# Optimization experiments

Hardware: AMD Instinct MI355X
Metric: run time of the kernel (lower is better)

Reference implementation:

```python
import jax, jax.numpy as jnp
import numpy as np

NEG = -10000.0
LN_EPS = 1e-5


def _longformer_attn(x, attn_val, Wq, bq, Wk, bk, Wv, bv, Wqg, bqg, Wkg, bkg, Wvg, bvg, w, H):
    # x: (B, S, D) with S % (2w) == 0; attn_val: (B, S) int, 0=local, -1=pad, +1=global (only last pos)
    B, S, D = x.shape
    d = D // H
    scale = float(1.0 / np.sqrt(d))
    q = (x @ Wq + bq).reshape(B, S, H, d) * scale
    k = (x @ Wk + bk).reshape(B, S, H, d)
    v = (x @ Wv + bv).reshape(B, S, H, d)
    g = S - 1                      # single global token (last position)
    C = S // w                     # number of query chunks of size w
    W3 = 3 * w
    # key/value windows: chunk c sees absolute keys [c*w - w, c*w + 2w)
    idx = np.arange(C)[:, None] * w + np.arange(W3)[None, :]           # (C, 3w) into padded length S+2w
    k_win = jnp.pad(k, ((0, 0), (w, w), (0, 0), (0, 0)))[:, idx]       # (B, C, 3w, H, d)
    v_win = jnp.pad(v, ((0, 0), (w, w), (0, 0), (0, 0)))[:, idx]
    qc = q.reshape(B, C, w, H, d)
    scores = jnp.einsum('bcxhd,bcyhd->bhcxy', qc, k_win)               # (B, H, C, w, 3w)
    # banded validity: relative offset in [-w, w] and absolute key index in [0, S)
    x_i = np.arange(w)[:, None]
    y_i = np.arange(W3)[None, :]
    rel_ok = (y_i - x_i >= 0) & (y_i - x_i <= 2 * w)                   # (w, 3w)
    j_abs = np.arange(C)[:, None, None] * w - w + y_i[None]            # (C, 1, 3w)
    valid = jnp.asarray(rel_ok[None] & ((j_abs >= 0) & (j_abs < S)))   # (C, w, 3w)
    # keys that are padding or global get -10000 inside the band (remove_from_windowed_attention_mask)
    rm_win = jnp.pad(attn_val != 0, ((0, 0), (w, w)))[:, idx]          # (B, C, 3w)
    scores = scores + jnp.where(rm_win, NEG, 0.0)[:, None, :, None, :]
    scores = jnp.where(valid[None, None], scores, -jnp.inf)
    # every query also attends to the global key (column prepended before softmax)
    g_scores = jnp.einsum('bcxhd,bhd->bhcx', qc, k[:, g])              # (B, H, C, w)
    all_s = jnp.concatenate([g_scores[..., None], scores], axis=-1)    # (B, H, C, w, 3w+1)
    probs = jax.nn.softmax(all_s, axis=-1)
    q_ok = (attn_val >= 0).astype(probs.dtype)                         # zero rows of padding queries
    probs = probs * q_ok.reshape(B, 1, C, w, 1)
    out = jnp.einsum('bhcxy,bcyhd->bcxhd', probs[..., 1:], v_win)
    out = out + jnp.einsum('bhcx,bhd->bcxhd', probs[..., 0], v[:, g])
    out = out.reshape(B, S, D)
    # global token: full attention over all keys with the *_global projections
    qg = (x[:, g] @ Wqg + bqg).reshape(B, H, d) * scale
    kg = (x @ Wkg + bkg).reshape(B, S, H, d)
    vg = (x @ Wvg + bvg).reshape(B, S, H, d)
    sg = jnp.einsum('bhd,bshd->bhs', qg, kg)
    sg = sg + jnp.where(attn_val < 0, NEG, 0.0)[:, None, :]
    og = jnp.einsum('bhs,bshd->bhd', jax.nn.softmax(sg, axis=-1), vg).reshape(B, D)
    return out.at[:, g].set(og)


def setup_inputs() -> dict:
    B, S, D, H, w, E = 2, 2048, 768, 12, 256, 4
    key = jax.random.key(0)
    ks = jax.random.split(key, 16)
    wmat = lambda k, s: jax.random.normal(k, s, dtype=jnp.float32) * 0.02
    inp = {
        'x': jax.random.normal(ks[0], (B, S, D), dtype=jnp.float32),
        'mask': jnp.ones((B, S), dtype=bool),
        'Wq': wmat(ks[1], (D, D)), 'bq': jnp.zeros((D,), jnp.float32),
        'Wk': wmat(ks[2], (D, D)), 'bk': jnp.zeros((D,), jnp.float32),
        'Wv': wmat(ks[3], (D, D)), 'bv': jnp.zeros((D,), jnp.float32),
        'Wqg': wmat(ks[4], (D, D)), 'bqg': jnp.zeros((D,), jnp.float32),
        'Wkg': wmat(ks[5], (D, D)), 'bkg': jnp.zeros((D,), jnp.float32),
        'Wvg': wmat(ks[6], (D, D)), 'bvg': jnp.zeros((D,), jnp.float32),
        'ln_g': jnp.ones((D,), jnp.float32), 'ln_b': jnp.zeros((D,), jnp.float32),
        'W1': wmat(ks[7], (D, E * D)), 'b1': jnp.zeros((E * D,), jnp.float32),
        'W2': wmat(ks[8], (E * D, D)), 'b2': jnp.zeros((D,), jnp.float32),
        'window_size': w,
        'num_heads': H,
    }
    return inp


def reference(x, mask, Wq, bq, Wk, bk, Wv, bv, Wqg, bqg, Wkg, bkg, Wvg, bvg,
              ln_g, ln_b, W1, b1, W2, b2, window_size, num_heads):
    B, S0, D = x.shape
    w = int(window_size)
    H = int(num_heads)
    pad = 2 * w - S0 % (2 * w)                          # always in [1, 2w], matches torch code
    xp = jnp.pad(x, ((0, 0), (0, pad), (0, 0)))         # pad_token_id = 0
    mp = jnp.pad(mask, ((0, 0), (0, pad)), constant_values=True)
    attn_val = mp.astype(jnp.int32) - 1                 # True->0 (local), False->-1 (pad)
    attn_val = attn_val.at[:, -1].set(1)                # last position is global
    xp = xp + _longformer_attn(xp, attn_val, Wq, bq, Wk, bk, Wv, bv,
                               Wqg, bqg, Wkg, bkg, Wvg, bvg, w, H)
    x1 = xp[:, :S0]
    mu = jnp.mean(x1, axis=-1, keepdims=True)
    var = jnp.mean((x1 - mu) ** 2, axis=-1, keepdims=True)
    xn = (x1 - mu) * jax.lax.rsqrt(var + LN_EPS) * ln_g + ln_b
    h = jax.nn.gelu(xn @ W1 + b1, approximate=False)
    return xn + h @ W2 + b2
```

## Files before the change

### kernel.cpp

```cpp
#include <hip/hip_runtime.h>
#include <hip/hip_bf16.h>

typedef unsigned short ushort_t;
typedef __attribute__((ext_vector_type(8))) __bf16 bf16x8;
typedef __attribute__((ext_vector_type(4))) float f32x4;
typedef __attribute__((ext_vector_type(4))) unsigned short us4;

#define S0 2048
#define DM 768
#define NH 12
#define DH 64
#define KS 2368
#define GK 2304

__device__ __forceinline__ float bf2f(ushort_t h){
  union{unsigned u; float f;} x; x.u = ((unsigned)h)<<16; return x.f;
}
__device__ __forceinline__ ushort_t f2bf(float f){
  union{float f; unsigned u;} x; x.f = f;
  unsigned r = (x.u + 0x7FFFu + ((x.u>>16)&1u))>>16;
  return (ushort_t)r;
}

typedef void as1_void __attribute__((address_space(1)));
typedef void as3_void __attribute__((address_space(3)));
__device__ __forceinline__ void lds_cp16(const void* g, void* s){
  __builtin_amdgcn_global_load_lds((as1_void*)g, (as3_void*)s, 16, 0, 0);
}

__device__ __forceinline__ int xcd_swizzle(int bid, int nwg){
  const int q8 = nwg>>3, r8 = nwg&7;
  const int xcd = bid & 7, sub = bid >> 3;
  return (xcd < r8 ? xcd*(q8+1) : r8*(q8+1) + (xcd-r8)*q8) + sub;
}

__global__ __launch_bounds__(256)
void prep_kernel(const float* __restrict__ Wq, const float* __restrict__ Wk,
                 const float* __restrict__ Wv, const float* __restrict__ W1,
                 const float* __restrict__ W2, const float* __restrict__ x,
                 const float* __restrict__ bq, const float* __restrict__ bk,
                 const float* __restrict__ bv,
                 ushort_t* __restrict__ WtQ, ushort_t* __restrict__ WtK,
                 ushort_t* __restrict__ WtV, ushort_t* __restrict__ Wt1,
                 ushort_t* __restrict__ Wt2, ushort_t* __restrict__ xb,
                 float* __restrict__ bqkv, ushort_t* __restrict__ Kb,
                 ushort_t* __restrict__ Vtb)
{
  __shared__ ushort_t tile[64][72];
  const int id = blockIdx.x, t = threadIdx.x;
  if (id < 1584){
    const float* src; ushort_t* dst; int K, N, bx, by;
    if (id < 432){
      const int m = id/144, r = id%144;
      src = (m==0)?Wq:((m==1)?Wk:Wv);
      dst = (m==0)?WtQ:((m==1)?WtK:WtV);
      K=768; N=768; bx=r%12; by=r/12;
    } else if (id < 1008){
      const int r = id-432; src=W1; dst=Wt1; K=768; N=3072; bx=r%48; by=r/48;
    } else {
      const int r = id-1008; src=W2; dst=Wt2; K=3072; N=768; bx=r%12; by=r/12;
    }
    const int n0 = bx*64, k0 = by*64;
    #pragma unroll
    for (int p=0; p<2; p++){
      int r = (t>>3) + p*32, c = (t&7)*8;
      const float* sp = src + (size_t)(k0+r)*N + n0 + c;
      const float4 a = *(const float4*)sp;
      const float4 b = *(const float4*)(sp+4);
      ushort_t v[8] = { f2bf(a.x), f2bf(a.y), f2bf(a.z), f2bf(a.w),
                        f2bf(b.x), f2bf(b.y), f2bf(b.z), f2bf(b.w) };
      *(int4*)&tile[r][c] = *(int4*)v;
    }
    __syncthreads();
    #pragma unroll
    for (int p=0; p<2; p++){
      int n = t&63, kc = (t>>6)*8 + p*32;
      ushort_t v[8];
      #pragma unroll
      for (int e=0; e<8; e++) v[e] = tile[kc+e][n];
      *(int4*)(dst + (size_t)(n0+n)*K + k0 + kc) = *(int4*)v;
    }
  } else if (id < 3120){
    const int i = (id-1584)*2048 + t*8;
    const float4 a = *(const float4*)(x+i);
    const float4 b = *(const float4*)(x+i+4);
    ushort_t v[8] = { f2bf(a.x), f2bf(a.y), f2bf(a.z), f2bf(a.w),
                      f2bf(b.x), f2bf(b.y), f2bf(b.z), f2bf(b.w) };
    *(int4*)(xb+i) = *(int4*)v;
  } else if (id < 3129){
    const int i = (id-3120)*256 + t;
    if (i < 2304)
      bqkv[i] = (i < 768) ? bq[i] : (i < 1536) ? bk[i-768] : bv[i-1536];
  } else if (id < 3369){
    const int i = (id-3129)*2048 + t*8;
    const int col = i % DM;
    const int rr  = i / DM;
    const int row = S0 + rr % (KS-S0);
    const int bb  = rr / (KS-S0);
    const float4 a = *(const float4*)(bk+col);
    const float4 b4 = *(const float4*)(bk+col+4);
    ushort_t v[8] = { f2bf(a.x), f2bf(a.y), f2bf(a.z), f2bf(a.w),
                      f2bf(b4.x), f2bf(b4.y), f2bf(b4.z), f2bf(b4.w) };
    *(int4*)&Kb[(size_t)bb*KS*DM + (size_t)row*DM + col] = *(int4*)v;
  } else {
    const int rid = id - 3369;
    const int h = (rid>>6) % NH;
    const int dd = rid & 63;
    const ushort_t val = f2bf(bv[h*64+dd]);
    if (t < 80){
      us4 pk = {val, val, val, val};
      *(us4*)&Vtb[(size_t)rid*KS + S0 + t*4] = pk;
    }
  }
}

template<int EPI, int NF, typename OT>
__global__ __launch_bounds__(256)
void gemm_bt(const ushort_t* __restrict__ A, const ushort_t* __restrict__ Bt,
             const float* __restrict__ bias, OT* __restrict__ C,
             ushort_t* __restrict__ C2, ushort_t* __restrict__ C3,
             int K, int ldc, long long ldcb, int nbx)
{
  __shared__ ushort_t As[128*64];
  __shared__ ushort_t Bs[NF*32*64];
  const int tid = threadIdx.x, wid = tid>>6, l = tid&63;

  const int wg = xcd_swizzle(blockIdx.x, gridDim.x);
  const int bx = wg % nbx, by = wg / nbx;
  const int m0 = by*128, n0 = bx*(NF*32);

  const int wm = wid>>1, wn = wid&1;
  const int lq = l&15, lg = l>>4;
  const int xa = lq&7;

  f32x4 acc[4][NF];
  const f32x4 zero = {0.f,0.f,0.f,0.f};
  #pragma unroll
  for (int i=0;i<4;i++)
    #pragma unroll
    for (int j=0;j<NF;j++) acc[i][j] = zero;

  const int swzc = ((l&7) ^ ((l>>3)&7)) * 8;
  const ushort_t* Ag = A  + (size_t)(m0 + wid*32 + (l>>3))*K + swzc;
  const ushort_t* Bg = Bt + (size_t)(n0 + wid*(NF*8) + (l>>3))*K + swzc;

  for (int k0=0; k0<K; k0+=64){
    #pragma unroll
    for (int i=0;i<4;i++)
      lds_cp16(Ag + (size_t)i*8*K + k0, As + wid*2048 + i*512);
    #pragma unroll
    for (int i=0;i<NF;i++)
      lds_cp16(Bg + (size_t)i*8*K + k0, Bs + wid*(NF*512) + i*512);
    __syncthreads();
    #pragma unroll
    for (int kk=0; kk<64; kk+=32){
      bf16x8 af[4], bfr[NF];
      #pragma unroll
      for (int mi=0;mi<4;mi++)
        af[mi] = *(const bf16x8*)&As[(wm*64+mi*16+lq)*64 + ((((kk>>3)+lg)^xa)<<3)];
      #pragma unroll
      for (int ni=0;ni<NF;ni++)
        bfr[ni] = *(const bf16x8*)&Bs[(wn*(NF*16)+ni*16+lq)*64 + ((((kk>>3)+lg)^xa)<<3)];
      #pragma unroll
      for (int mi=0;mi<4;mi++)
        #pragma unroll
        for (int ni=0;ni<NF;ni++)
          acc[mi][ni] = __builtin_amdgcn_mfma_f32_16x16x32_bf16(af[mi], bfr[ni], acc[mi][ni], 0,0,0);
    }
    __syncthreads();
  }

  if (EPI==4){
    const int seg = n0 / 768;
    if (seg == 2){
      #pragma unroll
      for (int mi=0;mi<4;mi++){
        const int mrow = m0 + wm*64 + mi*16 + lg*4;
        const int bb = mrow>>11, key = mrow&2047;
        #pragma unroll
        for (int ni=0;ni<NF;ni++){
          const int ncol = n0 + wn*(NF*16) + ni*16 + lq;
          const int col = ncol - 1536;
          const float bvv = bias[ncol];
          us4 pk;
          #pragma unroll
          for (int r=0;r<4;r++) pk[r] = f2bf(acc[mi][ni][r] + bvv);
          *(us4*)&C3[((size_t)(bb*NH + (col>>6))*64 + (col&63))*KS + key] = pk;
        }
      }
      return;
    }
    ushort_t* dst = (seg==0) ? (ushort_t*)C : C2;
    const long long bstride = (seg==1) ? (long long)KS*DM : 2048LL*DM;
    const float sc = (seg==0) ? 0.125f : 1.f;
    #pragma unroll
    for (int mi=0;mi<4;mi++){
      const int mrow = m0 + wm*64 + mi*16 + lg*4;
      #pragma unroll
      for (int ni=0;ni<NF;ni++){
        const int ncol = n0 + wn*(NF*16) + ni*16 + lq;
        const float bv = bias[ncol];
        const int col = ncol - seg*768;
        #pragma unroll
        for (int r=0;r<4;r++){
          const int m = mrow + r;
          const float v = (acc[mi][ni][r] + bv)*sc;
          dst[(size_t)((long long)(m>>11)*bstride) + (size_t)(m&2047)*DM + col] = f2bf(v);
        }
      }
    }
    return;
  }

  #pragma unroll
  for (int mi=0;mi<4;mi++){
    const int mrow = m0 + wm*64 + mi*16 + lg*4;
    #pragma unroll
    for (int ni=0;ni<NF;ni++){
      const int ncol = n0 + wn*(NF*16) + ni*16 + lq;
      const float bv = bias[ncol];
      #pragma unroll
      for (int r=0;r<4;r++){
        const int m = mrow + r;
        float v = acc[mi][ni][r] + bv;
        if (EPI==2) v = 0.5f*v*(1.f + erff(v*0.70710678118f));
        const size_t caddr = (size_t)((long long)(m>>11)*ldcb) + (size_t)(m&2047)*ldc + ncol;
        C[caddr] = f2bf(v);
      }
    }
  }
}

__global__ __launch_bounds__(256)
void gemm64_sk2(const ushort_t* __restrict__ A, const ushort_t* __restrict__ Bt,
                float* __restrict__ part)
{
  __shared__ ushort_t As[2][64*64];
  __shared__ ushort_t Bs[2][64*64];
  const int tid = threadIdx.x, wid = tid>>6, l = tid&63;

  const int wg = xcd_swizzle(blockIdx.x, gridDim.x);
  const int p = wg / 768, rem = wg % 768;
  const int bx = rem % 12, by = rem / 12;
  const int m0 = by*64, n0 = bx*64;
  const int kbeg = p*1536;

  const int wm = wid>>1, wn = wid&1;
  const int lq = l&15, lg = l>>4;
  const int xa = lq&7;

  f32x4 acc[2][2];
  const f32x4 zero = {0.f,0.f,0.f,0.f};
  acc[0][0]=zero; acc[0][1]=zero; acc[1][0]=zero; acc[1][1]=zero;

  const int swzc = ((l&7) ^ ((l>>3)&7)) * 8;
  const ushort_t* Ag = A  + (size_t)(m0 + wid*16 + (l>>3))*3072 + kbeg + swzc;
  const ushort_t* Bg = Bt + (size_t)(n0 + wid*16 + (l>>3))*3072 + kbeg + swzc;

  const int nk = 24;

  #pragma unroll
  for (int i=0;i<2;i++){
    lds_cp16(Ag + (size_t)i*8*3072, &As[0][wid*1024 + i*512]);
    lds_cp16(Bg + (size_t)i*8*3072, &Bs[0][wid*1024 + i*512]);
  }
  __syncthreads();

  for (int t=0; t<nk; ++t){
    const int cur = t&1;
    if (t+1 < nk){
      const int k0 = (t+1)<<6;
      #pragma unroll
      for (int i=0;i<2;i++){
        lds_cp16(Ag + (size_t)i*8*3072 + k0, &As[cur^1][wid*1024 + i*512]);
        lds_cp16(Bg + (size_t)i*8*3072 + k0, &Bs[cur^1][wid*1024 + i*512]);
      }
    }
    #pragma unroll
    for (int kk=0; kk<64; kk+=32){
      bf16x8 af[2], bfr[2];
      #pragma unroll
      for (int mi=0;mi<2;mi++)
        af[mi] = *(const bf16x8*)&As[cur][(wm*32+mi*16+lq)*64 + ((((kk>>3)+lg)^xa)<<3)];
      #pragma unroll
      for (int ni=0;ni<2;ni++)
        bfr[ni] = *(const bf16x8*)&Bs[cur][(wn*32+ni*16+lq)*64 + ((((kk>>3)+lg)^xa)<<3)];
      #pragma unroll
      for (int mi=0;mi<2;mi++)
        #pragma unroll
        for (int ni=0;ni<2;ni++)
          acc[mi][ni] = __builtin_amdgcn_mfma_f32_16x16x32_bf16(af[mi], bfr[ni], acc[mi][ni], 0,0,0);
    }
    __syncthreads();
  }

  float* dst = part + (size_t)p*4096*DM;
  #pragma unroll
  for (int mi=0;mi<2;mi++){
    const int mrow = m0 + wm*32 + mi*16 + lg*4;
    #pragma unroll
    for (int ni=0;ni<2;ni++){
      const int ncol = n0 + wn*32 + ni*16 + lq;
      #pragma unroll
      for (int r=0;r<4;r++)
        dst[(size_t)(mrow+r)*DM + ncol] = acc[mi][ni][r];
    }
  }
}

__global__ __launch_bounds__(256)
void ffn2_reduce(const float* __restrict__ part, const ushort_t* __restrict__ xn,
                 const float* __restrict__ b2, float* __restrict__ out)
{
  const int i = (blockIdx.x*256 + threadIdx.x)*8;
  const int col = i % DM;
  const float* p1 = part + (size_t)4096*DM;
  const float4 a0 = *(const float4*)(part + i);
  const float4 a1 = *(const float4*)(part + i + 4);
  const float4 c0 = *(const float4*)(p1 + i);
  const float4 c1 = *(const float4*)(p1 + i + 4);
  const us4 x0 = *(const us4*)(xn + i);
  const us4 x1 = *(const us4*)(xn + i + 4);
  const float4 b0 = *(const float4*)(b2 + col);
  const float4 b1 = *(const float4*)(b2 + col + 4);
  float4 o0, o1;
  o0.x = a0.x + c0.x + bf2f(x0[0]) + b0.x;
  o0.y = a0.y + c0.y + bf2f(x0[1]) + b0.y;
  o0.z = a0.z + c0.z + bf2f(x0[2]) + b0.z;
  o0.w = a0.w + c0.w + bf2f(x0[3]) + b0.w;
  o1.x = a1.x + c1.x + bf2f(x1[0]) + b1.x;
  o1.y = a1.y + c1.y + bf2f(x1[1]) + b1.y;
  o1.z = a1.z + c1.z + bf2f(x1[2]) + b1.z;
  o1.w = a1.w + c1.w + bf2f(x1[3]) + b1.w;
  *(float4*)(out + i)     = o0;
  *(float4*)(out + i + 4) = o1;
}

__global__ __launch_bounds__(512, 6)
void attn_kernel(const ushort_t* __restrict__ Q, const ushort_t* __restrict__ Kw,
                 const ushort_t* __restrict__ Vt, const float* __restrict__ x,
                 ushort_t* __restrict__ xattn)
{
  __shared__ ushort_t Ks[2][64*64];
  __shared__ ushort_t Vs[2][64*64];
  __shared__ ushort_t P_lds[8][16][72];
  const int t = threadIdx.x, w = t>>6, l = t&63;
  const int qb = blockIdx.x, bh = blockIdx.y;
  const int b = bh/NH, h = bh%NH;
  const int qs = qb*128 + w*16;
  const int lq = l&15, lg = l>>4;
  const int i_q = qs + lq;
  const int kwin0 = qb*128 - 256;

  const int lo = w*16 - 63;
  const int cmin = lo > 0 ? ((lo+63)>>6) : 0;
  int cmax = (w*16 + 527) >> 6; if (cmax > 9) cmax = 9;

  const ushort_t* Qp = Q  + ((size_t)b*S0 + qs)*DM + h*DH;
  const ushort_t* Kp = Kw + (size_t)b*KS*DM + h*DH;
  const ushort_t* Vp = Vt + (size_t)bh*DH*KS;

  const bf16x8 qf0 = *(const bf16x8*)(Qp + (size_t)lq*DM + lg*8);
  const bf16x8 qf1 = *(const bf16x8*)(Qp + (size_t)lq*DM + 32 + lg*8);

  const int rl = l>>3;
  const int sslot = (l&7) ^ rl;

  const f32x4 zero = {0.f,0.f,0.f,0.f};
  f32x4 accO[4];
  #pragma unroll
  for (int g=0; g<4; g++) accO[g] = zero;
  float lsum = 0.f;

  auto stage = [&](int c, int bf){
    const int kbase = kwin0 + c*64;
    const int ck = w*8 + rl;
    int krow = kbase + ck; if (krow < 0) krow = 0;
    lds_cp16(Kp + (size_t)krow*DM + sslot*8, &Ks[bf][(w*8)*64]);
    int kcol = kbase + sslot*8; if (kcol < 0) kcol = 0;
    lds_cp16(Vp + (size_t)ck*KS + kcol,      &Vs[bf][(w*8)*64]);
  };

  stage(0, 0);
  for (int c=0; c<10; ++c){
    __syncthreads();
    if (c+1 < 10) stage(c+1, (c+1)&1);
    if (c >= cmin && c <= cmax){
      const int cur = c&1;
      const int kbase = kwin0 + c*64;
      const bool fullv = (kbase >= 0) && (kbase + 63 < GK) &&
                         (kbase >= qs - 241) && (kbase <= qs + 193);
      const int slot0 = ((lg ^ (lq&7)) << 3);
      #pragma unroll
      for (int sb=0; sb<4; sb++){
        const bf16x8 kf0 = *(const bf16x8*)&Ks[cur][(sb*16+lq)*64 + slot0];
        const bf16x8 kf1 = *(const bf16x8*)&Ks[cur][(sb*16+lq)*64 + (slot0^32)];
        f32x4 s = zero;
        s = __builtin_amdgcn_mfma_f32_16x16x32_bf16(kf0, qf0, s, 0,0,0);
        s = __builtin_amdgcn_mfma_f32_16x16x32_bf16(kf1, qf1, s, 0,0,0);
        float pv[4];
        if (fullv){
          #pragma unroll
          for (int r=0; r<4; r++) pv[r] = __expf(s[r]);
        } else {
          #pragma unroll
          for (int r=0; r<4; r++){
            const int j = kbase + sb*16 + lg*4 + r;
            const bool valid = (j >= 0) && (j < GK) && (j >= i_q-256) && (j <= i_q+256);
            pv[r] = valid ? __expf(s[r]) : 0.f;
          }
        }
        lsum += (pv[0]+pv[1]) + (pv[2]+pv[3]);
        unsigned a0, a1;
        asm("v_cvt_pk_bf16_f32 %0, %1, %2" : "=v"(a0) : "v"(pv[0]), "v"(pv[1]));
        asm("v_cvt_pk_bf16_f32 %0, %1, %2" : "=v"(a1) : "v"(pv[2]), "v"(pv[3]));
        uint2 pk2; pk2.x = a0; pk2.y = a1;
        *(uint2*)&P_lds[w][lq][sb*16 + lg*4] = pk2;
      }
      #pragma unroll
      for (int r2=0; r2<2; r2++){
        const bf16x8 pf = *(const bf16x8*)&P_lds[w][lq][r2*32 + lg*8];
        #pragma unroll
        for (int g=0; g<4; g++){
          const int vslot = ((((r2<<2)|lg) ^ (lq&7)) << 3);
          const bf16x8 vtf = *(const bf16x8*)&Vs[cur][(g*16+lq)*64 + vslot];
          accO[g] = __builtin_amdgcn_mfma_f32_16x16x32_bf16(vtf, pf, accO[g], 0,0,0);
        }
      }
    }
  }

  {
    const ushort_t* kr = Kp + (size_t)(GK+lq)*DM + lg*8;
    const bf16x8 kf0 = *(const bf16x8*)(kr);
    const bf16x8 kf1 = *(const bf16x8*)(kr + 32);
    f32x4 s = zero;
    s = __builtin_amdgcn_mfma_f32_16x16x32_bf16(kf0, qf0, s, 0,0,0);
    s = __builtin_amdgcn_mfma_f32_16x16x32_bf16(kf1, qf1, s, 0,0,0);
    us4 pk, pz;
    #pragma unroll
    for (int r=0; r<4; r++){
      const float p = (lg==0 && r==0) ? __expf(s[r]) : 0.f;
      lsum += p;
      pk[r] = f2bf(p);
      pz[r] = 0;
    }
    *(us4*)&P_lds[w][lq][lg*4] = pk;
    *(us4*)&P_lds[w][lq][16 + lg*4] = pz;
    const bf16x8 pf = *(const bf16x8*)&P_lds[w][lq][lg*8];
    const int kb_lane = GK + (lg&1)*8;
    #pragma unroll
    for (int g=0; g<4; g++){
      const bf16x8 vtf = *(const bf16x8*)(Vp + (size_t)(g*16 + lq)*KS + kb_lane);
      accO[g] = __builtin_amdgcn_mfma_f32_16x16x32_bf16(vtf, pf, accO[g], 0,0,0);
    }
  }

  lsum += __shfl_xor(lsum, 16);
  lsum += __shfl_xor(lsum, 32);
  const float inv = 1.f / lsum;

  const float* xr = x + ((size_t)b*S0 + i_q)*DM + h*DH;
  ushort_t* outp = xattn + ((size_t)b*S0 + i_q)*DM + h*DH;
  #pragma unroll
  for (int g=0; g<4; g++){
    const float4 xv = *(const float4*)(xr + g*16 + lg*4);
    us4 o;
    o[0] = f2bf(accO[g][0]*inv + xv.x);
    o[1] = f2bf(accO[g][1]*inv + xv.y);
    o[2] = f2bf(accO[g][2]*inv + xv.z);
    o[3] = f2bf(accO[g][3]*inv + xv.w);
    *(us4*)(outp + g*16 + lg*4) = o;
  }
}

__global__ __launch_bounds__(192)
void ln_kernel(const ushort_t* __restrict__ xattn, const float* __restrict__ gam,
               const float* __restrict__ bet, ushort_t* __restrict__ xn)
{
  const int row = blockIdx.x, t = threadIdx.x;
  const us4 xv = *(const us4*)(xattn + (size_t)row*DM + t*4);
  float v[4];
  float s = 0.f, ss = 0.f;
  #pragma unroll
  for (int r=0;r<4;r++){ v[r] = bf2f(xv[r]); s += v[r]; ss += v[r]*v[r]; }
  #pragma unroll
  for (int o=1; o<64; o<<=1){ s += __shfl_xor(s,o); ss += __shfl_xor(ss,o); }
  __shared__ float red[3][2];
  if ((t&63)==0){ red[t>>6][0]=s; red[t>>6][1]=ss; }
  __syncthreads();
  const float S  = red[0][0]+red[1][0]+red[2][0];
  const float SS = red[0][1]+red[1][1]+red[2][1];
  const float mu = S*(1.f/768.f);
  const float var = SS*(1.f/768.f) - mu*mu;
  const float rs = rsqrtf(var + 1e-5f);
  const float4 g4 = *(const float4*)(gam + t*4);
  const float4 b4 = *(const float4*)(bet + t*4);
  us4 o;
  o[0] = f2bf((v[0]-mu)*rs*g4.x + b4.x);
  o[1] = f2bf((v[1]-mu)*rs*g4.y + b4.y);
  o[2] = f2bf((v[2]-mu)*rs*g4.z + b4.z);
  o[3] = f2bf((v[3]-mu)*rs*g4.w + b4.w);
  *(us4*)(xn + (size_t)row*DM + t*4) = o;
}

extern "C" void kernel_launch(void* const* d_in, const int* in_sizes, int n_in,
                              void* d_out, int out_size, void* d_ws, size_t ws_size,
                              hipStream_t stream)
{
  const float* x   = (const float*)d_in[0];
  const float* Wq  = (const float*)d_in[2];
  const float* bq  = (const float*)d_in[3];
  const float* Wk  = (const float*)d_in[4];
  const float* bk  = (const float*)d_in[5];
  const float* Wv  = (const float*)d_in[6];
  const float* bv  = (const float*)d_in[7];
  const float* lng = (const float*)d_in[14];
  const float* lnb = (const float*)d_in[15];
  const float* W1  = (const float*)d_in[16];
  const float* b1  = (const float*)d_in[17];
  const float* W2  = (const float*)d_in[18];
  const float* b2  = (const float*)d_in[19];
  float* out = (float*)d_out;

  char* ws = (char*)d_ws;
  ushort_t* xb  = (ushort_t*)(ws + 0);
  ushort_t* Qb  = (ushort_t*)(ws + 6291456);
  ushort_t* Kb  = (ushort_t*)(ws + 12582912);
  ushort_t* Vtb = (ushort_t*)(ws + 19857408);
  ushort_t* hb  = (ushort_t*)(ws + 0);
  size_t o2 = 27131904;
  ushort_t* WtQ = (ushort_t*)(ws + o2); o2 += 1179648;
  ushort_t* WtK = (ushort_t*)(ws + o2); o2 += 1179648;
  ushort_t* WtV = (ushort_t*)(ws + o2); o2 += 1179648;
  ushort_t* Wt1 = (ushort_t*)(ws + o2); o2 += 4718592;
  ushort_t* Wt2 = (ushort_t*)(ws + o2); o2 += 4718592;
  ushort_t* xat = (ushort_t*)(ws + o2); o2 += 6291456;
  ushort_t* xnb = (ushort_t*)(ws + o2); o2 += 6291456;
  float*    bqkv= (float*)   (ws + o2); o2 += 9216;
  float*    part= (float*)   (ws + o2); o2 += 25165824;
  (void)ws_size; (void)in_sizes; (void)n_in; (void)out_size;

  prep_kernel<<<4905,256,0,stream>>>(Wq, Wk, Wv, W1, W2, x, bq, bk, bv,
                                     WtQ, WtK, WtV, Wt1, Wt2, xb, bqkv, Kb, Vtb);

  gemm_bt<4,3,ushort_t><<<768,256,0,stream>>>(xb, WtQ, bqkv, Qb, Kb, Vtb,
                                              768, 768, 0LL, 24);

  attn_kernel<<<dim3(16,24),512,0,stream>>>(Qb, Kb, Vtb, x, xat);

  ln_kernel<<<4096,192,0,stream>>>(xat, lng, lnb, xnb);

  gemm_bt<2,3,ushort_t><<<1024,256,0,stream>>>(xnb, Wt1, b1, hb, nullptr, nullptr,
                                               768, 3072, 2048LL*3072, 32);
  gemm64_sk2<<<1536,256,0,stream>>>(hb, Wt2, part);
  ffn2_reduce<<<1536,256,0,stream>>>(part, xnb, b2, out);
}
```

Baseline: 151.4 us.

## Retile FFN GEMMs and drop double buffering in split-K and attention kernels

The FFN2 split-K GEMM moves from 64x64 to 128x64 tiles, halving its grid, and goes from double-buffered LDS to single-buffered loads with a sync per K step. The attention kernel likewise drops K/V double buffering and adds an extra barrier after each chunk. The FFN1 GEMM switches to a narrower N tile and a larger grid. The intent is to raise occupancy and per-block reuse by cutting LDS use, at the cost of no longer overlapping global loads with MFMA work.

```diff
diff --git a/kernel.cpp b/kernel.cpp
--- a/kernel.cpp
+++ b/kernel.cpp
@@ -232,61 +232,51 @@
 }
 
 __global__ __launch_bounds__(256)
-void gemm64_sk2(const ushort_t* __restrict__ A, const ushort_t* __restrict__ Bt,
-                float* __restrict__ part)
-{
-  __shared__ ushort_t As[2][64*64];
-  __shared__ ushort_t Bs[2][64*64];
+void gemm_sk(const ushort_t* __restrict__ A, const ushort_t* __restrict__ Bt,
+             float* __restrict__ part)
+{
+  __shared__ ushort_t As[128*64];
+  __shared__ ushort_t Bs[64*64];
   const int tid = threadIdx.x, wid = tid>>6, l = tid&63;
 
   const int wg = xcd_swizzle(blockIdx.x, gridDim.x);
-  const int p = wg / 768, rem = wg % 768;
+  const int p = wg / 384, rem = wg % 384;
   const int bx = rem % 12, by = rem / 12;
-  const int m0 = by*64, n0 = bx*64;
+  const int m0 = by*128, n0 = bx*64;
   const int kbeg = p*1536;
 
   const int wm = wid>>1, wn = wid&1;
   const int lq = l&15, lg = l>>4;
   const int xa = lq&7;
 
-  f32x4 acc[2][2];
+  f32x4 acc[4][2];
   const f32x4 zero = {0.f,0.f,0.f,0.f};
-  acc[0][0]=zero; acc[0][1]=zero; acc[1][0]=zero; acc[1][1]=zero;
+  #pragma unroll
+  for (int i=0;i<4;i++){ acc[i][0]=zero; acc[i][1]=zero; }
 
   const int swzc = ((l&7) ^ ((l>>3)&7)) * 8;
-  const ushort_t* Ag = A  + (size_t)(m0 + wid*16 + (l>>3))*3072 + kbeg + swzc;
+  const ushort_t* Ag = A  + (size_t)(m0 + wid*32 + (l>>3))*3072 + kbeg + swzc;
   const ushort_t* Bg = Bt + (size_t)(n0 + wid*16 + (l>>3))*3072 + kbeg + swzc;
 
-  const int nk = 24;
-
-  #pragma unroll
-  for (int i=0;i<2;i++){
-    lds_cp16(Ag + (size_t)i*8*3072, &As[0][wid*1024 + i*512]);
-    lds_cp16(Bg + (size_t)i*8*3072, &Bs[0][wid*1024 + i*512]);
-  }
-  __syncthreads();
-
-  for (int t=0; t<nk; ++t){
-    const int cur = t&1;
-    if (t+1 < nk){
-      const int k0 = (t+1)<<6;
-      #pragma unroll
-      for (int i=0;i<2;i++){
-        lds_cp16(Ag + (size_t)i*8*3072 + k0, &As[cur^1][wid*1024 + i*512]);
-        lds_cp16(Bg + (size_t)i*8*3072 + k0, &Bs[cur^1][wid*1024 + i*512]);
-      }
-    }
+  for (int k0=0; k0<1536; k0+=64){
+    #pragma unroll
+    for (int i=0;i<4;i++)
+      lds_cp16(Ag + (size_t)i*8*3072 + k0, As + wid*2048 + i*512);
+    #pragma unroll
+    for (int i=0;i<2;i++)
+      lds_cp16(Bg + (size_t)i*8*3072 + k0, Bs + wid*1024 + i*512);
+    __syncthreads();
     #pragma unroll
     for (int kk=0; kk<64; kk+=32){
-      bf16x8 af[2], bfr[2];
-      #pragma unroll
-      for (int mi=0;mi<2;mi++)
-        af[mi] = *(const bf16x8*)&As[cur][(wm*32+mi*16+lq)*64 + ((((kk>>3)+lg)^xa)<<3)];
+      bf16x8 af[4], bfr[2];
+      #pragma unroll
+      for (int mi=0;mi<4;mi++)
+        af[mi] = *(const bf16x8*)&As[(wm*64+mi*16+lq)*64 + ((((kk>>3)+lg)^xa)<<3)];
       #pragma unroll
       for (int ni=0;ni<2;ni++)
-        bfr[ni] = *(const bf16x8*)&Bs[cur][(wn*32+ni*16+lq)*64 + ((((kk>>3)+lg)^xa)<<3)];
-      #pragma unroll
-      for (int mi=0;mi<2;mi++)
+        bfr[ni] = *(const bf16x8*)&Bs[(wn*32+ni*16+lq)*64 + ((((kk>>3)+lg)^xa)<<3)];
+      #pragma unroll
+      for (int mi=0;mi<4;mi++)
         #pragma unroll
         for (int ni=0;ni<2;ni++)
           acc[mi][ni] = __builtin_amdgcn_mfma_f32_16x16x32_bf16(af[mi], bfr[ni], acc[mi][ni], 0,0,0);
@@ -296,8 +286,8 @@
 
   float* dst = part + (size_t)p*4096*DM;
   #pragma unroll
-  for (int mi=0;mi<2;mi++){
-    const int mrow = m0 + wm*32 + mi*16 + lg*4;
+  for (int mi=0;mi<4;mi++){
+    const int mrow = m0 + wm*64 + mi*16 + lg*4;
     #pragma unroll
     for (int ni=0;ni<2;ni++){
       const int ncol = n0 + wn*32 + ni*16 + lq;
@@ -341,8 +331,8 @@
                  const ushort_t* __restrict__ Vt, const float* __restrict__ x,
                  ushort_t* __restrict__ xattn)
 {
-  __shared__ ushort_t Ks[2][64*64];
-  __shared__ ushort_t Vs[2][64*64];
+  __shared__ ushort_t Ks[64*64];
+  __shared__ ushort_t Vs[64*64];
   __shared__ ushort_t P_lds[8][16][72];
   const int t = threadIdx.x, w = t>>6, l = t&63;
   const int qb = blockIdx.x, bh = blockIdx.y;
@@ -372,29 +362,27 @@
   for (int g=0; g<4; g++) accO[g] = zero;
   float lsum = 0.f;
 
-  auto stage = [&](int c, int bf){
+  auto stage = [&](int c){
     const int kbase = kwin0 + c*64;
     const int ck = w*8 + rl;
     int krow = kbase + ck; if (krow < 0) krow = 0;
-    lds_cp16(Kp + (size_t)krow*DM + sslot*8, &Ks[bf][(w*8)*64]);
+    lds_cp16(Kp + (size_t)krow*DM + sslot*8, &Ks[(w*8)*64]);
     int kcol = kbase + sslot*8; if (kcol < 0) kcol = 0;
-    lds_cp16(Vp + (size_t)ck*KS + kcol,      &Vs[bf][(w*8)*64]);
+    lds_cp16(Vp + (size_t)ck*KS + kcol,      &Vs[(w*8)*64]);
   };
 
-  stage(0, 0);
+  stage(0);
+  __syncthreads();
   for (int c=0; c<10; ++c){
-    __syncthreads();
-    if (c+1 < 10) stage(c+1, (c+1)&1);
     if (c >= cmin && c <= cmax){
-      const int cur = c&1;
       const int kbase = kwin0 + c*64;
       const bool fullv = (kbase >= 0) && (kbase + 63 < GK) &&
                          (kbase >= qs - 241) && (kbase <= qs + 193);
       const int slot0 = ((lg ^ (lq&7)) << 3);
       #pragma unroll
       for (int sb=0; sb<4; sb++){
-        const bf16x8 kf0 = *(const bf16x8*)&Ks[cur][(sb*16+lq)*64 + slot0];
-        const bf16x8 kf1 = *(const bf16x8*)&Ks[cur][(sb*16+lq)*64 + (slot0^32)];
+        const bf16x8 kf0 = *(const bf16x8*)&Ks[(sb*16+lq)*64 + slot0];
+        const bf16x8 kf1 = *(const bf16x8*)&Ks[(sb*16+lq)*64 + (slot0^32)];
         f32x4 s = zero;
         s = __builtin_amdgcn_mfma_f32_16x16x32_bf16(kf0, qf0, s, 0,0,0);
         s = __builtin_amdgcn_mfma_f32_16x16x32_bf16(kf1, qf1, s, 0,0,0);
@@ -423,10 +411,15 @@
         #pragma unroll
         for (int g=0; g<4; g++){
           const int vslot = ((((r2<<2)|lg) ^ (lq&7)) << 3);
-          const bf16x8 vtf = *(const bf16x8*)&Vs[cur][(g*16+lq)*64 + vslot];
+          const bf16x8 vtf = *(const bf16x8*)&Vs[(g*16+lq)*64 + vslot];
           accO[g] = __builtin_amdgcn_mfma_f32_16x16x32_bf16(vtf, pf, accO[g], 0,0,0);
         }
       }
+    }
+    __syncthreads();
+    if (c+1 < 10){
+      stage(c+1);
+      __syncthreads();
     }
   }
 
@@ -551,8 +544,8 @@
 
   ln_kernel<<<4096,192,0,stream>>>(xat, lng, lnb, xnb);
 
-  gemm_bt<2,3,ushort_t><<<1024,256,0,stream>>>(xnb, Wt1, b1, hb, nullptr, nullptr,
-                                               768, 3072, 2048LL*3072, 32);
-  gemm64_sk2<<<1536,256,0,stream>>>(hb, Wt2, part);
+  gemm_bt<2,2,ushort_t><<<1536,256,0,stream>>>(xnb, Wt1, b1, hb, nullptr, nullptr,
+                                               768, 3072, 2048LL*3072, 48);
+  gemm_sk<<<768,256,0,stream>>>(hb, Wt2, part);
   ffn2_reduce<<<1536,256,0,stream>>>(part, xnb, b2, out);
 }
```

Result: faster. 140.0 us (-7.6%).
